# Performance work log

Hardware: AMD Instinct MI355X
Metric: run time of the kernel (lower is better)

Reference implementation:

```python
import jax, jax.numpy as jnp
import numpy as np

B, L, DIM, H = 1, 2048, 3072, 24
D = DIM // H  # 128
EPS = 1e-6

def setup_inputs() -> dict:
    key = jax.random.key(0)
    ks = jax.random.split(key, 7)
    x = jax.random.normal(ks[0], (B, L, DIM), dtype=jnp.float32)
    pe = jax.random.normal(ks[1], (B, 1, L, D // 2, 2, 2), dtype=jnp.float32)
    w_qkv = jax.random.normal(ks[2], (DIM, 3 * DIM), dtype=jnp.float32) / np.sqrt(DIM)
    q_scale = jnp.ones((D,), dtype=jnp.float32)
    k_scale = jnp.ones((D,), dtype=jnp.float32)
    w_proj = jax.random.normal(ks[3], (DIM, DIM), dtype=jnp.float32) / np.sqrt(DIM)
    b_proj = jnp.zeros((DIM,), dtype=jnp.float32)
    return {"x": x, "pe": pe, "w_qkv": w_qkv, "q_scale": q_scale,
            "k_scale": k_scale, "w_proj": w_proj, "b_proj": b_proj}

def _rmsnorm(t, scale):
    # flax nn.RMSNorm: t * rsqrt(mean(t^2, -1) + eps) * scale
    ms = jnp.mean(jnp.square(t), axis=-1, keepdims=True)
    return t * jax.lax.rsqrt(ms + EPS) * scale

def _apply_rope(xq, xk, pe):
    # xq/xk: [B,H,L,D]; pe: [B,1,L,D/2,2,2]
    xq_ = xq.reshape(*xq.shape[:-1], -1, 1, 2)
    xk_ = xk.reshape(*xk.shape[:-1], -1, 1, 2)
    xq_out = pe[..., 0] * xq_[..., 0] + pe[..., 1] * xq_[..., 1]
    xk_out = pe[..., 0] * xk_[..., 0] + pe[..., 1] * xk_[..., 1]
    return xq_out.reshape(xq.shape), xk_out.reshape(xk.shape)

def reference(x, pe, w_qkv, q_scale, k_scale, w_proj, b_proj):
    qkv = jnp.einsum('bld,de->ble', x, w_qkv)            # [B,L,3*DIM]
    qkv = qkv.reshape(B, L, 3, H, D)
    qkv = jnp.moveaxis(qkv, 2, 0)                          # [3,B,H?,..]
    q, k, v = jnp.transpose(qkv, (0, 1, 3, 2, 4))          # each [B,H,L,D]
    q = _rmsnorm(q, q_scale).astype(v.dtype)
    k = _rmsnorm(k, k_scale).astype(v.dtype)
    q, k = _apply_rope(q, k, pe)
    scale = 1.0 / np.sqrt(D)
    scores = jnp.einsum('bhqd,bhkd->bhqk', q, k) * scale   # [B,H,L,L]
    attn = jax.nn.softmax(scores, axis=-1)
    out = jnp.einsum('bhqk,bhkd->bhqd', attn, v)           # [B,H,L,D]
    out = jnp.transpose(out, (0, 2, 1, 3)).reshape(B, L, DIM)
    return jnp.einsum('bld,de->ble', out, w_proj) + b_proj
```

## Files before the change

### kernel.cpp

```cpp
#include <hip/hip_runtime.h>

#define L_    2048
#define DIM_  3072
#define H_    24
#define D_    128
#define NQKV  9216

typedef __attribute__((ext_vector_type(8))) short bf16x8;
typedef __attribute__((ext_vector_type(4))) short bf16x4;
typedef __attribute__((ext_vector_type(4))) float f32x4;

__device__ __forceinline__ unsigned short f2bf(float f) {
  union { float f; unsigned u; } v; v.f = f;
  unsigned r = v.u + 0x7fffu + ((v.u >> 16) & 1u);
  return (unsigned short)(r >> 16);
}

__device__ __forceinline__ void gload_lds16(const void* g, void* l) {
  auto* lp = reinterpret_cast<__attribute__((address_space(3))) unsigned int*>(
      reinterpret_cast<uintptr_t>(l));
  auto* gp = reinterpret_cast<const __attribute__((address_space(1))) unsigned int*>(
      reinterpret_cast<uintptr_t>(g));
  __builtin_amdgcn_global_load_lds(gp, lp, 16, 0, 0);
}

__global__ void cast_f32_to_bf16(const float* __restrict__ in,
                                 unsigned short* __restrict__ out, int n) {
  int total = n >> 2;
  int stride = gridDim.x * blockDim.x;
  for (int i = blockIdx.x * blockDim.x + threadIdx.x; i < total; i += stride) {
    float4 v = ((const float4*)in)[i];
    ushort4 o;
    o.x = f2bf(v.x); o.y = f2bf(v.y); o.z = f2bf(v.z); o.w = f2bf(v.w);
    ((ushort4*)out)[i] = o;
  }
}

__global__ __launch_bounds__(256)
void castT_f32_bf16(const float* __restrict__ in, unsigned short* __restrict__ out,
                    int K, int N) {
  const int tid  = threadIdx.x;
  const int lane = tid & 63;
  const int wave = tid >> 6;
  const int nq = lane & 7;
  const int kq = lane >> 3;
  const int k0 = blockIdx.x * 128 + (wave & 1) * 64 + kq * 8;
  const int n0 = blockIdx.y * 64  + (wave >> 1) * 32 + nq * 4;
  float4 v[8];
  #pragma unroll
  for (int i = 0; i < 8; i++)
    v[i] = *(const float4*)&in[(size_t)(k0 + i) * N + n0];
  #pragma unroll
  for (int j = 0; j < 4; j++) {
    bf16x8 o;
    #pragma unroll
    for (int i = 0; i < 8; i++)
      o[i] = (short)f2bf(((const float*)&v[i])[j]);
    *(bf16x8*)&out[(size_t)(n0 + j) * K + k0] = o;
  }
}

__global__ __launch_bounds__(256, 3)
void gemm_qkv(const unsigned short* __restrict__ A,
              const unsigned short* __restrict__ Bt,
              const float* __restrict__ pe,
              const float* __restrict__ q_scale,
              const float* __restrict__ k_scale,
              unsigned short* __restrict__ Qo,
              unsigned short* __restrict__ Ko,
              unsigned short* __restrict__ Vt)
{
  const int K = DIM_;
  __shared__ __align__(16) unsigned short S[128 * 132];
  unsigned short* As = S;
  unsigned short* Bs = S + 128 * 64;
  const int tid  = threadIdx.x;
  const int wave = tid >> 6;
  const int lane = tid & 63;
  const int l15  = lane & 15;
  const int quad = lane >> 4;
  const int wm = wave >> 1, wn = wave & 1;

  const int lin = blockIdx.x;
  const int st  = lin >> 6;
  const int w6  = lin & 63;
  const int bn_idx = (st >> 1) * 8 + (w6 & 7);
  const int bm_idx = (st & 1) * 8 + (w6 >> 3);
  const int bm = bm_idx * 128;
  const int bn = bn_idx * 128;

  const int srow = lane >> 3;
  const int scol = (lane & 7) ^ srow;
  const unsigned short* Ag = A  + (size_t)(bm + wave * 32 + srow) * K + scol * 8;
  const unsigned short* Bg = Bt + (size_t)(bn + wave * 32 + srow) * K + scol * 8;
  unsigned short* Al = &As[(wave * 32) * 64];
  unsigned short* Bl = &Bs[(wave * 32) * 64];

  f32x4 acc[4][4];
  #pragma unroll
  for (int i = 0; i < 4; i++)
    #pragma unroll
    for (int j = 0; j < 4; j++) acc[i][j] = (f32x4){0.f, 0.f, 0.f, 0.f};

  for (int k0 = 0; k0 < K; k0 += 64) {
    __syncthreads();
    #pragma unroll
    for (int j = 0; j < 4; j++) {
      gload_lds16(Ag + (size_t)j * 8 * K + k0, Al + j * 8 * 64);
      gload_lds16(Bg + (size_t)j * 8 * K + k0, Bl + j * 8 * 64);
    }
    __syncthreads();
    #pragma unroll
    for (int ks = 0; ks < 2; ks++) {
      const int cph = ((ks * 4 + quad) ^ (l15 & 7)) * 8;
      bf16x8 af[4], bf[4];
      #pragma unroll
      for (int mt = 0; mt < 4; mt++)
        af[mt] = *(const bf16x8*)&As[(wm * 64 + mt * 16 + l15) * 64 + cph];
      #pragma unroll
      for (int nt = 0; nt < 4; nt++)
        bf[nt] = *(const bf16x8*)&Bs[(wn * 64 + nt * 16 + l15) * 64 + cph];
      #pragma unroll
      for (int mt = 0; mt < 4; mt++)
        #pragma unroll
        for (int nt = 0; nt < 4; nt++)
          acc[mt][nt] = __builtin_amdgcn_mfma_f32_16x16x32_bf16(
              af[mt], bf[nt], acc[mt][nt], 0, 0, 0);
    }
  }
  __syncthreads();

  if (bn_idx < 48) {
    const bool isQ = bn_idx < 24;
    const int  hh  = isQ ? bn_idx : bn_idx - 24;
    const float* sc = isQ ? q_scale : k_scale;
    unsigned short* dst = isQ ? Qo : Ko;
    float* rbuf = (float*)S;
    #pragma unroll
    for (int mt = 0; mt < 4; mt++)
      #pragma unroll
      for (int r = 0; r < 4; r++) {
        float p = 0.f;
        #pragma unroll
        for (int nt = 0; nt < 4; nt++) p += acc[mt][nt][r] * acc[mt][nt][r];
        p += __shfl_xor(p, 1); p += __shfl_xor(p, 2);
        p += __shfl_xor(p, 4); p += __shfl_xor(p, 8);
        if (l15 == 0) rbuf[wn * 128 + wm * 64 + mt * 16 + quad * 4 + r] = p;
      }
    __syncthreads();
    #pragma unroll
    for (int mt = 0; mt < 4; mt++)
      #pragma unroll
      for (int r = 0; r < 4; r++) {
        const int lrow = wm * 64 + mt * 16 + quad * 4 + r;
        const int lg = bm + lrow;
        float ms = (rbuf[lrow] + rbuf[128 + lrow]) * (1.f / 128.f);
        float rinv = rsqrtf(ms + 1e-6f);
        #pragma unroll
        for (int nt = 0; nt < 4; nt++) {
          const int d = wn * 64 + nt * 16 + l15;
          float n  = acc[mt][nt][r] * rinv * sc[d];
          float np = __shfl_xor(n, 1);
          float2 ab = *(const float2*)&pe[(size_t)lg * 256 + (d >> 1) * 4 + (d & 1) * 2];
          float xe = (d & 1) ? np : n;
          float xo = (d & 1) ? n  : np;
          float o = ab.x * xe + ab.y * xo;
          if (isQ) o *= 0.08838834764831845f;
          dst[((size_t)hh * L_ + lg) * D_ + d] = f2bf(o);
        }
      }
  } else {
    const int hh = bn_idx - 48;
    unsigned short (*St)[132] = (unsigned short(*)[132])S;
    #pragma unroll
    for (int mt = 0; mt < 4; mt++)
      #pragma unroll
      for (int nt = 0; nt < 4; nt++)
        #pragma unroll
        for (int r = 0; r < 4; r++) {
          int row = wm * 64 + mt * 16 + quad * 4 + r;
          int col = wn * 64 + nt * 16 + l15;
          St[row][col] = f2bf(acc[mt][nt][r]);
        }
    __syncthreads();
    const int grp = tid >> 6;
    const int ll  = tid & 63;
    unsigned short* dstV = Vt + (size_t)hh * D_ * L_;
    #pragma unroll
    for (int dd = 0; dd < 32; dd += 4) {
      const int d = grp * 32 + dd;
      #pragma unroll
      for (int half = 0; half < 2; half++) {
        const int l = ll + half * 64;
        bf16x4 v4 = *(const bf16x4*)&St[l][d];
        #pragma unroll
        for (int j = 0; j < 4; j++)
          dstV[(size_t)(d + j) * L_ + bm + l] = ((const unsigned short*)&v4)[j];
      }
    }
  }
}

__global__ __launch_bounds__(256, 3)
void gemm_proj_sk(const unsigned short* __restrict__ A,
                  const unsigned short* __restrict__ Bt,
                  float* __restrict__ P0, float* __restrict__ P1,
                  int M, int N, int K)
{
  __shared__ unsigned short As[128 * 64];
  __shared__ unsigned short Bs[128 * 64];
  const int tid  = threadIdx.x;
  const int wave = tid >> 6;
  const int lane = tid & 63;
  const int l15  = lane & 15;
  const int quad = lane >> 4;
  const int wm = wave >> 1, wn = wave & 1;
  const int bm = blockIdx.y * 128;
  const int bn = blockIdx.x * 128;
  const int z  = blockIdx.z;
  const int kbeg = z * (K >> 1), kend = kbeg + (K >> 1);
  float* Pout = z ? P1 : P0;

  const int srow = lane >> 3;
  const int scol = (lane & 7) ^ srow;
  const unsigned short* Ag = A  + (size_t)(bm + wave * 32 + srow) * K + scol * 8;
  const unsigned short* Bg = Bt + (size_t)(bn + wave * 32 + srow) * K + scol * 8;
  unsigned short* Al = &As[(wave * 32) * 64];
  unsigned short* Bl = &Bs[(wave * 32) * 64];

  f32x4 acc[4][4];
  #pragma unroll
  for (int i = 0; i < 4; i++)
    #pragma unroll
    for (int j = 0; j < 4; j++) acc[i][j] = (f32x4){0.f, 0.f, 0.f, 0.f};

  for (int k0 = kbeg; k0 < kend; k0 += 64) {
    __syncthreads();
    #pragma unroll
    for (int j = 0; j < 4; j++) {
      gload_lds16(Ag + (size_t)j * 8 * K + k0, Al + j * 8 * 64);
      gload_lds16(Bg + (size_t)j * 8 * K + k0, Bl + j * 8 * 64);
    }
    __syncthreads();
    #pragma unroll
    for (int ks = 0; ks < 2; ks++) {
      const int cph = ((ks * 4 + quad) ^ (l15 & 7)) * 8;
      bf16x8 af[4], bf[4];
      #pragma unroll
      for (int mt = 0; mt < 4; mt++)
        af[mt] = *(const bf16x8*)&As[(wm * 64 + mt * 16 + l15) * 64 + cph];
      #pragma unroll
      for (int nt = 0; nt < 4; nt++)
        bf[nt] = *(const bf16x8*)&Bs[(wn * 64 + nt * 16 + l15) * 64 + cph];
      #pragma unroll
      for (int mt = 0; mt < 4; mt++)
        #pragma unroll
        for (int nt = 0; nt < 4; nt++)
          acc[mt][nt] = __builtin_amdgcn_mfma_f32_16x16x32_bf16(
              af[mt], bf[nt], acc[mt][nt], 0, 0, 0);
    }
  }
  #pragma unroll
  for (int mt = 0; mt < 4; mt++)
    #pragma unroll
    for (int nt = 0; nt < 4; nt++)
      #pragma unroll
      for (int r = 0; r < 4; r++) {
        int row = bm + wm * 64 + mt * 16 + quad * 4 + r;
        int col = bn + wn * 64 + nt * 16 + l15;
        Pout[(size_t)row * N + col] = acc[mt][nt][r];
      }
}

__global__ __launch_bounds__(256)
void reduce_bias(const float* __restrict__ p0, const float* __restrict__ p1,
                 const float* __restrict__ bias, float* __restrict__ out)
{
  int col4 = blockIdx.x * 256 + threadIdx.x;
  size_t idx = (size_t)blockIdx.y * 768 + col4;
  float4 a = ((const float4*)p0)[idx];
  float4 b = ((const float4*)p1)[idx];
  float4 c = ((const float4*)bias)[col4];
  float4 o = make_float4(a.x + b.x + c.x, a.y + b.y + c.y,
                         a.z + b.z + c.z, a.w + b.w + c.w);
  ((float4*)out)[idx] = o;
}

__global__ __launch_bounds__(256, 3)
void flash_attn(const unsigned short* __restrict__ Q,
                const unsigned short* __restrict__ K,
                const unsigned short* __restrict__ Vt,
                unsigned short* __restrict__ Out)
{
  __shared__ __align__(16) char smem[49152];
  float*  Obuf = (float*)smem;
  float2* mlb  = (float2*)(smem + 32768);
  float4* sAr  = (float4*)(smem + 33280);

  const int tid  = threadIdx.x;
  const int wave = tid >> 6;
  const int lane = tid & 63;
  const int l15  = lane & 15;
  const int quad = lane >> 4;
  const int qg = wave >> 1;
  const int kh = wave & 1;
  const int id   = blockIdx.x;
  const int slot = id >> 3;
  const int h    = (id & 7) * 3 + slot % 3;
  const int q0   = (slot / 3) * 64 + qg * 32;

  const unsigned short* Qh = Q  + (size_t)h * L_ * D_;
  const unsigned short* Kh = K  + (size_t)h * L_ * D_;
  const unsigned short* Vh = Vt + (size_t)h * D_ * L_;

  bf16x8 qf[2][4];
  #pragma unroll
  for (int nt = 0; nt < 2; nt++)
    #pragma unroll
    for (int kc = 0; kc < 4; kc++)
      qf[nt][kc] = *(const bf16x8*)&Qh[(size_t)(q0 + nt * 16 + l15) * D_ + kc * 32 + quad * 8];

  f32x4 oacc[2][8];
  #pragma unroll
  for (int i = 0; i < 2; i++)
    #pragma unroll
    for (int j = 0; j < 8; j++) oacc[i][j] = (f32x4){0.f, 0.f, 0.f, 0.f};
  float m_i[2] = {-1e30f, -1e30f}, l_i[2] = {0.f, 0.f};

  const int kr_l = lane >> 4;
  const int vr_l = lane >> 3;
  const int vcl  = (lane & 7) ^ vr_l;

  auto stageK = [&](int t, int b) {
    unsigned short* Ksb = (unsigned short*)(smem + b * 16384);
    #pragma unroll
    for (int ji = 0; ji < 4; ji++) {
      int Rr = wave * 16 + ji * 4;
      int cl = l15 ^ ((Rr + kr_l) & 15);
      gload_lds16(&Kh[(size_t)(t + Rr + kr_l) * D_ + cl * 8], &Ksb[Rr * 128]);
    }
  };
  auto stageV = [&](int t) {
    unsigned short* Vsb = (unsigned short*)(smem + 32768);
    #pragma unroll
    for (int ji = 0; ji < 4; ji++) {
      int R2 = wave * 32 + ji * 8;
      gload_lds16(&Vh[(size_t)(R2 + vr_l) * L_ + t + vcl * 8], &Vsb[R2 * 64]);
    }
  };

  stageK(0, 0);
  stageV(0);

  for (int t = 0; t < L_; t += 64) {
    const int cur = (t >> 6) & 1;
    const bool more = (t + 64 < L_);

    asm volatile("s_waitcnt vmcnt(4)" ::: "memory");
    __builtin_amdgcn_s_barrier();
    if (more) stageK(t + 64, cur ^ 1);

    const unsigned short* Ksc = (const unsigned short*)(smem + cur * 16384);
    const unsigned short* Vsc = (const unsigned short*)(smem + 32768);

    f32x4 s[2][2];
    #pragma unroll
    for (int i = 0; i < 2; i++)
      #pragma unroll
      for (int j = 0; j < 2; j++) s[i][j] = (f32x4){0.f, 0.f, 0.f, 0.f};
    __builtin_amdgcn_s_setprio(1);
    #pragma unroll
    for (int mt = 0; mt < 2; mt++) {
      const int krow = kh * 32 + mt * 16 + l15;
      #pragma unroll
      for (int kc = 0; kc < 4; kc++) {
        bf16x8 kf = *(const bf16x8*)&Ksc[krow * 128 + (((kc * 4 + quad) ^ l15) * 8)];
        s[mt][0] = __builtin_amdgcn_mfma_f32_16x16x32_bf16(kf, qf[0][kc], s[mt][0], 0, 0, 0);
        s[mt][1] = __builtin_amdgcn_mfma_f32_16x16x32_bf16(kf, qf[1][kc], s[mt][1], 0, 0, 0);
      }
    }
    __builtin_amdgcn_s_setprio(0);

    float vmax[2];
    #pragma unroll
    for (int nt = 0; nt < 2; nt++) {
      vmax[nt] = fmaxf(fmaxf(fmaxf(s[0][nt][0], s[0][nt][1]), fmaxf(s[0][nt][2], s[0][nt][3])),
                       fmaxf(fmaxf(s[1][nt][0], s[1][nt][1]), fmaxf(s[1][nt][2], s[1][nt][3])));
      vmax[nt] = fmaxf(vmax[nt], __shfl_xor(vmax[nt], 16));
      vmax[nt] = fmaxf(vmax[nt], __shfl_xor(vmax[nt], 32));
    }
    if (!__all((vmax[0] - m_i[0] <= 8.f) && (vmax[1] - m_i[1] <= 8.f))) {
      float alpha[2];
      #pragma unroll
      for (int nt = 0; nt < 2; nt++) {
        float mnew = fmaxf(m_i[nt], vmax[nt]);
        alpha[nt] = __expf(m_i[nt] - mnew);
        m_i[nt] = mnew;
        l_i[nt] *= alpha[nt];
      }
      float ar[2][4];
      #pragma unroll
      for (int qt = 0; qt < 2; qt++)
        #pragma unroll
        for (int r = 0; r < 4; r++)
          ar[qt][r] = __shfl(alpha[qt], quad * 4 + r);
      #pragma unroll
      for (int qt = 0; qt < 2; qt++)
        #pragma unroll
        for (int ntd = 0; ntd < 8; ntd++)
          #pragma unroll
          for (int r = 0; r < 4; r++)
            oacc[qt][ntd][r] *= ar[qt][r];
    }
    float rs[2] = {0.f, 0.f};
    #pragma unroll
    for (int mt = 0; mt < 2; mt++)
      #pragma unroll
      for (int nt = 0; nt < 2; nt++)
        #pragma unroll
        for (int r = 0; r < 4; r++) {
          float p = __expf(s[mt][nt][r] - m_i[nt]);
          s[mt][nt][r] = p;
          rs[nt] += p;
        }
    #pragma unroll
    for (int nt = 0; nt < 2; nt++) {
      rs[nt] += __shfl_xor(rs[nt], 16);
      rs[nt] += __shfl_xor(rs[nt], 32);
      l_i[nt] += rs[nt];
    }
    bf16x4 pk[2][2];
    #pragma unroll
    for (int mt = 0; mt < 2; mt++)
      #pragma unroll
      for (int qt = 0; qt < 2; qt++)
        pk[mt][qt] = (bf16x4){(short)f2bf(s[mt][qt][0]), (short)f2bf(s[mt][qt][1]),
                              (short)f2bf(s[mt][qt][2]), (short)f2bf(s[mt][qt][3])};

    if (more) asm volatile("s_waitcnt vmcnt(4)" ::: "memory");
    else      asm volatile("s_waitcnt vmcnt(0)" ::: "memory");
    __builtin_amdgcn_s_barrier();

    __builtin_amdgcn_s_setprio(1);
    #pragma unroll
    for (int ntd = 0; ntd < 8; ntd++) {
      const int vrow = ntd * 16 + l15;
      #pragma unroll
      for (int mt = 0; mt < 2; mt++) {
        int phys = (kh * 4 + mt * 2 + (quad >> 1)) ^ (l15 & 7);
        bf16x4 vf = *(const bf16x4*)&Vsc[vrow * 64 + phys * 8 + (quad & 1) * 4];
        oacc[0][ntd] = __builtin_amdgcn_mfma_f32_16x16x16bf16_1k(pk[mt][0], vf, oacc[0][ntd], 0, 0, 0);
        oacc[1][ntd] = __builtin_amdgcn_mfma_f32_16x16x16bf16_1k(pk[mt][1], vf, oacc[1][ntd], 0, 0, 0);
      }
    }
    __builtin_amdgcn_s_setprio(0);

    if (more) {
      __builtin_amdgcn_s_barrier();
      stageV(t + 64);
    }
  }

  __syncthreads();
  if (kh == 1) {
    #pragma unroll
    for (int qt = 0; qt < 2; qt++)
      #pragma unroll
      for (int ntd = 0; ntd < 8; ntd++)
        #pragma unroll
        for (int r = 0; r < 4; r++)
          Obuf[(size_t)(qg * 32 + qt * 16 + quad * 4 + r) * 128 + ntd * 16 + l15] = oacc[qt][ntd][r];
    if (quad == 0)
      #pragma unroll
      for (int qt = 0; qt < 2; qt++)
        mlb[qg * 32 + qt * 16 + l15] = make_float2(m_i[qt], l_i[qt]);
  }
  __syncthreads();
  if (kh == 0 && quad == 0) {
    #pragma unroll
    for (int qt = 0; qt < 2; qt++) {
      float2 m1 = mlb[qg * 32 + qt * 16 + l15];
      float M  = fmaxf(m_i[qt], m1.x);
      float a0 = __expf(m_i[qt] - M);
      float a1 = __expf(m1.x - M);
      float Ls = l_i[qt] * a0 + m1.y * a1;
      sAr[qg * 32 + qt * 16 + l15] = make_float4(a0, a1, 1.f / Ls, 0.f);
    }
  }
  __syncthreads();
  if (kh == 0) {
    #pragma unroll
    for (int qt = 0; qt < 2; qt++)
      #pragma unroll
      for (int r = 0; r < 4; r++) {
        float4 A = sAr[qg * 32 + qt * 16 + quad * 4 + r];
        #pragma unroll
        for (int ntd = 0; ntd < 8; ntd++) {
          float o1 = Obuf[(size_t)(qg * 32 + qt * 16 + quad * 4 + r) * 128 + ntd * 16 + l15];
          float v  = (oacc[qt][ntd][r] * A.x + o1 * A.y) * A.z;
          Out[(size_t)(q0 + qt * 16 + quad * 4 + r) * DIM_ + h * D_ + ntd * 16 + l15] = f2bf(v);
        }
      }
  }
}

extern "C" void kernel_launch(void* const* d_in, const int* in_sizes, int n_in,
                              void* d_out, int out_size, void* d_ws, size_t ws_size,
                              hipStream_t stream) {
  const float* x       = (const float*)d_in[0];
  const float* pe      = (const float*)d_in[1];
  const float* w_qkv   = (const float*)d_in[2];
  const float* q_scale = (const float*)d_in[3];
  const float* k_scale = (const float*)d_in[4];
  const float* w_proj  = (const float*)d_in[5];
  const float* b_proj  = (const float*)d_in[6];

  unsigned short* w_qkvT  = (unsigned short*)d_ws;
  unsigned short* w_projT = w_qkvT + 28311552;
  unsigned short* x_b     = w_projT + 9437184;
  unsigned short* v_buf   = x_b + 6291456;
  unsigned short* q_r     = v_buf + 6291456;
  unsigned short* k_r     = q_r + 6291456;
  unsigned short* vt_r    = k_r + 6291456;
  unsigned short* attn_b  = vt_r + 6291456;
  float* proj_p0 = (float*)x_b;
  float* proj_p1 = (float*)q_r;

  cast_f32_to_bf16<<<2048, 256, 0, stream>>>(x, x_b, 6291456);
  castT_f32_bf16<<<dim3(24, 144), 256, 0, stream>>>(w_qkv, w_qkvT, 3072, 9216);
  castT_f32_bf16<<<dim3(24, 48), 256, 0, stream>>>(w_proj, w_projT, 3072, 3072);

  gemm_qkv<<<1152, 256, 0, stream>>>(
      x_b, w_qkvT, pe, q_scale, k_scale, q_r, k_r, vt_r);

  flash_attn<<<768, 256, 0, stream>>>(q_r, k_r, vt_r, attn_b);

  gemm_proj_sk<<<dim3(24, 16, 2), 256, 0, stream>>>(
      attn_b, w_projT, proj_p0, proj_p1, 2048, 3072, 3072);

  reduce_bias<<<dim3(3, 2048), 256, 0, stream>>>(
      proj_p0, proj_p1, b_proj, (float*)d_out);
}
```

Measured before the change: 524.0 us.

## Fold log2e into Q scale, use exp2, fuse weight casts, swizzle proj grid

The Q scale now includes log2(e), so the attention softmax can use exp2f instead of __expf. The rescale threshold is adjusted to match the base-2 domain, and P is packed to bf16 with the hardware v_cvt_pk_bf16_f32 instruction. The two weight-transpose casts are merged into one launch, and the projection GEMM grid is remapped into 8x8 tile groups for better L2 reuse. This cuts ALU work in the softmax and launch overhead, at the cost of slightly different bf16 rounding (the packed convert may round differently from the manual RNE).

```diff
diff --git a/kernel.cpp b/kernel.cpp
--- a/kernel.cpp
+++ b/kernel.cpp
@@ -37,26 +37,31 @@
 }
 
 __global__ __launch_bounds__(256)
-void castT_f32_bf16(const float* __restrict__ in, unsigned short* __restrict__ out,
-                    int K, int N) {
+void castT_two(const float* __restrict__ in0, unsigned short* __restrict__ out0,
+               const float* __restrict__ in1, unsigned short* __restrict__ out1) {
+  const int K = 3072;
+  int by = blockIdx.y;
+  const float* in; unsigned short* out; int N, n0;
+  if (by < 144) { in = in0; out = out0; N = 9216; n0 = by * 64; }
+  else          { in = in1; out = out1; N = 3072; n0 = (by - 144) * 64; }
   const int tid  = threadIdx.x;
   const int lane = tid & 63;
   const int wave = tid >> 6;
   const int nq = lane & 7;
   const int kq = lane >> 3;
   const int k0 = blockIdx.x * 128 + (wave & 1) * 64 + kq * 8;
-  const int n0 = blockIdx.y * 64  + (wave >> 1) * 32 + nq * 4;
+  const int nb = n0 + (wave >> 1) * 32 + nq * 4;
   float4 v[8];
   #pragma unroll
   for (int i = 0; i < 8; i++)
-    v[i] = *(const float4*)&in[(size_t)(k0 + i) * N + n0];
+    v[i] = *(const float4*)&in[(size_t)(k0 + i) * N + nb];
   #pragma unroll
   for (int j = 0; j < 4; j++) {
     bf16x8 o;
     #pragma unroll
     for (int i = 0; i < 8; i++)
       o[i] = (short)f2bf(((const float*)&v[i])[j]);
-    *(bf16x8*)&out[(size_t)(n0 + j) * K + k0] = o;
+    *(bf16x8*)&out[(size_t)(nb + j) * K + k0] = o;
   }
 }
 
@@ -165,7 +170,7 @@
           float xe = (d & 1) ? np : n;
           float xo = (d & 1) ? n  : np;
           float o = ab.x * xe + ab.y * xo;
-          if (isQ) o *= 0.08838834764831845f;
+          if (isQ) o *= (0.08838834764831845f * 1.4426950408889634f);
           dst[((size_t)hh * L_ + lg) * D_ + d] = f2bf(o);
         }
       }
@@ -215,9 +220,12 @@
   const int l15  = lane & 15;
   const int quad = lane >> 4;
   const int wm = wave >> 1, wn = wave & 1;
-  const int bm = blockIdx.y * 128;
-  const int bn = blockIdx.x * 128;
-  const int z  = blockIdx.z;
+  const int lin = blockIdx.x;
+  const int st  = lin >> 6;
+  const int w6  = lin & 63;
+  const int bn = ((st >> 1) * 8 + (w6 & 7)) * 128;
+  const int bm = ((st & 1) * 8 + (w6 >> 3)) * 128;
+  const int z  = blockIdx.y;
   const int kbeg = z * (K >> 1), kend = kbeg + (K >> 1);
   float* Pout = z ? P1 : P0;
 
@@ -384,17 +392,19 @@
     float vmax[2];
     #pragma unroll
     for (int nt = 0; nt < 2; nt++) {
-      vmax[nt] = fmaxf(fmaxf(fmaxf(s[0][nt][0], s[0][nt][1]), fmaxf(s[0][nt][2], s[0][nt][3])),
-                       fmaxf(fmaxf(s[1][nt][0], s[1][nt][1]), fmaxf(s[1][nt][2], s[1][nt][3])));
-      vmax[nt] = fmaxf(vmax[nt], __shfl_xor(vmax[nt], 16));
-      vmax[nt] = fmaxf(vmax[nt], __shfl_xor(vmax[nt], 32));
-    }
-    if (!__all((vmax[0] - m_i[0] <= 8.f) && (vmax[1] - m_i[1] <= 8.f))) {
+      float a = fmaxf(fmaxf(s[0][nt][0], s[0][nt][1]), s[0][nt][2]);
+      a = fmaxf(fmaxf(a, s[0][nt][3]), s[1][nt][0]);
+      a = fmaxf(fmaxf(a, s[1][nt][1]), s[1][nt][2]);
+      a = fmaxf(a, s[1][nt][3]);
+      a = fmaxf(a, __shfl_xor(a, 16));
+      vmax[nt] = fmaxf(a, __shfl_xor(a, 32));
+    }
+    if (!__all((vmax[0] - m_i[0] <= 11.5415603f) && (vmax[1] - m_i[1] <= 11.5415603f))) {
       float alpha[2];
       #pragma unroll
       for (int nt = 0; nt < 2; nt++) {
         float mnew = fmaxf(m_i[nt], vmax[nt]);
-        alpha[nt] = __expf(m_i[nt] - mnew);
+        alpha[nt] = exp2f(m_i[nt] - mnew);
         m_i[nt] = mnew;
         l_i[nt] *= alpha[nt];
       }
@@ -419,7 +429,7 @@
       for (int nt = 0; nt < 2; nt++)
         #pragma unroll
         for (int r = 0; r < 4; r++) {
-          float p = __expf(s[mt][nt][r] - m_i[nt]);
+          float p = exp2f(s[mt][nt][r] - m_i[nt]);
           s[mt][nt][r] = p;
           rs[nt] += p;
         }
@@ -433,9 +443,14 @@
     #pragma unroll
     for (int mt = 0; mt < 2; mt++)
       #pragma unroll
-      for (int qt = 0; qt < 2; qt++)
-        pk[mt][qt] = (bf16x4){(short)f2bf(s[mt][qt][0]), (short)f2bf(s[mt][qt][1]),
-                              (short)f2bf(s[mt][qt][2]), (short)f2bf(s[mt][qt][3])};
+      for (int qt = 0; qt < 2; qt++) {
+        union { unsigned int u2[2]; bf16x4 v4; } pku;
+        asm("v_cvt_pk_bf16_f32 %0, %1, %2"
+            : "=v"(pku.u2[0]) : "v"(s[mt][qt][0]), "v"(s[mt][qt][1]));
+        asm("v_cvt_pk_bf16_f32 %0, %1, %2"
+            : "=v"(pku.u2[1]) : "v"(s[mt][qt][2]), "v"(s[mt][qt][3]));
+        pk[mt][qt] = pku.v4;
+      }
 
     if (more) asm volatile("s_waitcnt vmcnt(4)" ::: "memory");
     else      asm volatile("s_waitcnt vmcnt(0)" ::: "memory");
@@ -481,8 +496,8 @@
     for (int qt = 0; qt < 2; qt++) {
       float2 m1 = mlb[qg * 32 + qt * 16 + l15];
       float M  = fmaxf(m_i[qt], m1.x);
-      float a0 = __expf(m_i[qt] - M);
-      float a1 = __expf(m1.x - M);
+      float a0 = exp2f(m_i[qt] - M);
+      float a1 = exp2f(m1.x - M);
       float Ls = l_i[qt] * a0 + m1.y * a1;
       sAr[qg * 32 + qt * 16 + l15] = make_float4(a0, a1, 1.f / Ls, 0.f);
     }
@@ -518,24 +533,22 @@
   unsigned short* w_qkvT  = (unsigned short*)d_ws;
   unsigned short* w_projT = w_qkvT + 28311552;
   unsigned short* x_b     = w_projT + 9437184;
-  unsigned short* v_buf   = x_b + 6291456;
-  unsigned short* q_r     = v_buf + 6291456;
+  unsigned short* q_r     = x_b + 6291456;
   unsigned short* k_r     = q_r + 6291456;
   unsigned short* vt_r    = k_r + 6291456;
   unsigned short* attn_b  = vt_r + 6291456;
   float* proj_p0 = (float*)x_b;
-  float* proj_p1 = (float*)q_r;
+  float* proj_p1 = (float*)k_r;
 
   cast_f32_to_bf16<<<2048, 256, 0, stream>>>(x, x_b, 6291456);
-  castT_f32_bf16<<<dim3(24, 144), 256, 0, stream>>>(w_qkv, w_qkvT, 3072, 9216);
-  castT_f32_bf16<<<dim3(24, 48), 256, 0, stream>>>(w_proj, w_projT, 3072, 3072);
+  castT_two<<<dim3(24, 192), 256, 0, stream>>>(w_qkv, w_qkvT, w_proj, w_projT);
 
   gemm_qkv<<<1152, 256, 0, stream>>>(
       x_b, w_qkvT, pe, q_scale, k_scale, q_r, k_r, vt_r);
 
   flash_attn<<<768, 256, 0, stream>>>(q_r, k_r, vt_r, attn_b);
 
-  gemm_proj_sk<<<dim3(24, 16, 2), 256, 0, stream>>>(
+  gemm_proj_sk<<<dim3(384, 2), 256, 0, stream>>>(
       attn_b, w_projT, proj_p0, proj_p1, 2048, 3072, 3072);
 
   reduce_bias<<<dim3(3, 2048), 256, 0, stream>>>(
```

Measured after the change: 504.7 us. -3.7%, faster.
